# Kernel tuning notes

Measured on AMD Instinct MI355X. Metric: run time of the kernel, lower is better.

Reference implementation:

```python
import jax, jax.numpy as jnp
import numpy as np

B, T, D = 64, 4096, 512

def setup_inputs() -> dict:
    key = jax.random.key(0)
    k1, k2 = jax.random.split(key)
    x = jax.random.normal(k1, (B, T, D), dtype=jnp.float32)
    W = jax.random.normal(k2, (D, 1), dtype=jnp.float32)
    b = jnp.zeros((T, 1), dtype=jnp.float32)
    return {"x": x, "W": W, "b": b}

def reference(x, W, b):
    # e: [B, T, 1] = tanh(x @ W + b), b broadcast over batch
    e = jnp.tanh(jnp.einsum('btd,do->bto', x, W) + b)
    a = jax.nn.softmax(e, axis=1)          # softmax over time axis
    return jnp.sum(a * x, axis=1)          # [B, D]
```

## Files before the change

### kernel.cpp

```cpp
#include <hip/hip_runtime.h>
#include <math.h>

#define Bsz 64
#define Tsz 4096
#define Dsz 512
#define ROWS 32
#define THREADS 512
#define CHUNKS (Tsz / ROWS)

__global__ __launch_bounds__(THREADS) void attn_phase1(
    const float* __restrict__ x, const float* __restrict__ W,
    const float* __restrict__ bias, float* __restrict__ num,
    float* __restrict__ den) {
  __shared__ float xs[ROWS * Dsz];
  __shared__ float wrow[ROWS];

  const int tid  = threadIdx.x;
  const int lane = tid & 63;
  const int wave = tid >> 6;
  const int s = blockIdx.x;
  const int b = blockIdx.y;

  const float* src = x + ((size_t)b * Tsz + (size_t)s * ROWS) * Dsz;

  float Wreg[8];
#pragma unroll
  for (int k = 0; k < 8; ++k) Wreg[k] = W[lane + 64 * k];

  {
    const float4* s4 = (const float4*)src;
    float4* l4 = (float4*)xs;
#pragma unroll
    for (int it = 0; it < 8; ++it)
      l4[it * THREADS + tid] = s4[it * THREADS + tid];
  }
  __syncthreads();

#pragma unroll
  for (int q = 0; q < 4; ++q) {
    const int r = wave + 8 * q;
    const float* xr = xs + r * Dsz;
    float p = 0.f;
#pragma unroll
    for (int k = 0; k < 8; ++k) p += xr[lane + 64 * k] * Wreg[k];
#pragma unroll
    for (int off = 32; off >= 1; off >>= 1) p += __shfl_xor(p, off, 64);
    if (lane == 0) {
      float e = tanhf(p + bias[s * ROWS + r]);
      wrow[r] = expf(e);
    }
  }
  __syncthreads();

  if (wave == 0) {
    float dv = (lane < ROWS) ? wrow[lane] : 0.f;
#pragma unroll
    for (int off = 32; off >= 1; off >>= 1) dv += __shfl_xor(dv, off, 64);
    if (lane == 0) atomicAdd(&den[b], dv);
  }

  float acc = 0.f;
#pragma unroll
  for (int t = 0; t < ROWS; ++t) acc += wrow[t] * xs[t * Dsz + tid];
  atomicAdd(&num[(size_t)b * Dsz + tid], acc);
}

__global__ __launch_bounds__(512) void attn_phase2(
    const float* __restrict__ num, const float* __restrict__ den,
    float* __restrict__ out) {
  const int i = blockIdx.x * blockDim.x + threadIdx.x;
  const int b = i >> 9;
  out[i] = num[i] / den[b];
}

extern "C" void kernel_launch(void* const* d_in, const int* in_sizes, int n_in,
                              void* d_out, int out_size, void* d_ws, size_t ws_size,
                              hipStream_t stream) {
  const float* x    = (const float*)d_in[0];
  const float* W    = (const float*)d_in[1];
  const float* bias = (const float*)d_in[2];
  float* num = (float*)d_ws;
  float* den = num + (size_t)Bsz * Dsz;

  hipMemsetAsync(d_ws, 0, ((size_t)Bsz * Dsz + Bsz) * sizeof(float), stream);

  dim3 g1(CHUNKS, Bsz);
  attn_phase1<<<g1, THREADS, 0, stream>>>(x, W, bias, num, den);
  attn_phase2<<<Bsz, Dsz, 0, stream>>>(num, den, (float*)d_out);
}
```

Baseline: 690.5 us.

## Stream rows per wave in registers instead of staging chunk in LDS

Each wave now owns 16 consecutive rows and loads them straight into registers as float4, computing the dot product, tanh/exp weight and weighted accumulation in one pass with no LDS staging of x. Partial sums per wave are reduced through a small shared buffer, then atomically added to global. Blocks shrink to 256 threads covering 64 rows, so there are half as many atomics per element. The goal is to drop the 64KB LDS tile, which limited occupancy, and the extra LDS read pass. The trade-off is a serial per-wave loop with shuffle reductions on every row.

```diff
diff --git a/kernel.cpp b/kernel.cpp
--- a/kernel.cpp
+++ b/kernel.cpp
@@ -4,65 +4,75 @@
 #define Bsz 64
 #define Tsz 4096
 #define Dsz 512
-#define ROWS 32
-#define THREADS 512
-#define CHUNKS (Tsz / ROWS)
+
+#define THREADS 256
+#define NWAVES (THREADS / 64)
+#define ROWS_PER_WAVE 16
+#define CH (NWAVES * ROWS_PER_WAVE)
+#define CHUNKS (Tsz / CH)
 
 __global__ __launch_bounds__(THREADS) void attn_phase1(
     const float* __restrict__ x, const float* __restrict__ W,
     const float* __restrict__ bias, float* __restrict__ num,
     float* __restrict__ den) {
-  __shared__ float xs[ROWS * Dsz];
-  __shared__ float wrow[ROWS];
-
   const int tid  = threadIdx.x;
   const int lane = tid & 63;
   const int wave = tid >> 6;
   const int s = blockIdx.x;
   const int b = blockIdx.y;
 
-  const float* src = x + ((size_t)b * Tsz + (size_t)s * ROWS) * Dsz;
+  const float4* W4 = (const float4*)W;
+  const float4 w0 = W4[2 * lane];
+  const float4 w1 = W4[2 * lane + 1];
 
-  float Wreg[8];
+  const int row0 = s * CH + wave * ROWS_PER_WAVE;
+  const float4* xr = (const float4*)(x + ((size_t)b * Tsz + row0) * Dsz);
+  const float* brow = bias + row0;
+
+  float4 acc0 = make_float4(0.f, 0.f, 0.f, 0.f);
+  float4 acc1 = make_float4(0.f, 0.f, 0.f, 0.f);
+  float wsum = 0.f;
+
+#pragma unroll 2
+  for (int i = 0; i < ROWS_PER_WAVE; ++i) {
+    const float4 a0 = xr[(size_t)i * (Dsz / 4) + 2 * lane];
+    const float4 a1 = xr[(size_t)i * (Dsz / 4) + 2 * lane + 1];
+    const float bi = brow[i];
+
+    float p = a0.x * w0.x + a0.y * w0.y + a0.z * w0.z + a0.w * w0.w
+            + a1.x * w1.x + a1.y * w1.y + a1.z * w1.z + a1.w * w1.w;
 #pragma unroll
-  for (int k = 0; k < 8; ++k) Wreg[k] = W[lane + 64 * k];
+    for (int off = 32; off >= 1; off >>= 1) p += __shfl_xor(p, off, 64);
 
-  {
-    const float4* s4 = (const float4*)src;
-    float4* l4 = (float4*)xs;
-#pragma unroll
-    for (int it = 0; it < 8; ++it)
-      l4[it * THREADS + tid] = s4[it * THREADS + tid];
+    const float wgt = expf(tanhf(p + bi));
+    wsum += wgt;
+    acc0.x += wgt * a0.x; acc0.y += wgt * a0.y;
+    acc0.z += wgt * a0.z; acc0.w += wgt * a0.w;
+    acc1.x += wgt * a1.x; acc1.y += wgt * a1.y;
+    acc1.z += wgt * a1.z; acc1.w += wgt * a1.w;
   }
+
+  __shared__ float red[NWAVES][Dsz];
+  __shared__ float redw[NWAVES];
+  float4* dst = (float4*)&red[wave][0];
+  dst[2 * lane]     = acc0;
+  dst[2 * lane + 1] = acc1;
+  if (lane == 0) redw[wave] = wsum;
   __syncthreads();
 
 #pragma unroll
-  for (int q = 0; q < 4; ++q) {
-    const int r = wave + 8 * q;
-    const float* xr = xs + r * Dsz;
-    float p = 0.f;
+  for (int c = tid; c < Dsz; c += THREADS) {
+    float v = 0.f;
 #pragma unroll
-    for (int k = 0; k < 8; ++k) p += xr[lane + 64 * k] * Wreg[k];
+    for (int wv = 0; wv < NWAVES; ++wv) v += red[wv][c];
+    atomicAdd(&num[(size_t)b * Dsz + c], v);
+  }
+  if (tid == 0) {
+    float dv = 0.f;
 #pragma unroll
-    for (int off = 32; off >= 1; off >>= 1) p += __shfl_xor(p, off, 64);
-    if (lane == 0) {
-      float e = tanhf(p + bias[s * ROWS + r]);
-      wrow[r] = expf(e);
-    }
+    for (int wv = 0; wv < NWAVES; ++wv) dv += redw[wv];
+    atomicAdd(&den[b], dv);
   }
-  __syncthreads();
-
-  if (wave == 0) {
-    float dv = (lane < ROWS) ? wrow[lane] : 0.f;
-#pragma unroll
-    for (int off = 32; off >= 1; off >>= 1) dv += __shfl_xor(dv, off, 64);
-    if (lane == 0) atomicAdd(&den[b], dv);
-  }
-
-  float acc = 0.f;
-#pragma unroll
-  for (int t = 0; t < ROWS; ++t) acc += wrow[t] * xs[t * Dsz + tid];
-  atomicAdd(&num[(size_t)b * Dsz + tid], acc);
 }
 
 __global__ __launch_bounds__(512) void attn_phase2(
```

Result: faster. 673.6 us (-2.4%).
